# Kernel tuning notes

Hardware: AMD Instinct MI355X
Metric: run time of the kernel (lower is better)

The kernel has to match this reference:

```python
import jax, jax.numpy as jnp
import numpy as np

H = 8   # n_heads
C = 2   # top-k scale factor: topk = int(C * log(L))


def setup_inputs() -> dict:
    key = jax.random.key(0)
    k1, k2, k3 = jax.random.split(key, 3)
    B, L, D = 16, 512, 4096  # L == D // H required by the original broadcasting
    Q = jax.random.normal(k1, (B, L, D), dtype=jnp.float32)
    K = jax.random.normal(k2, (B, L, D), dtype=jnp.float32)
    V = jax.random.normal(k3, (B, L, D), dtype=jnp.float32)
    return {"Q": Q, "K": K, "V": V}


def _autocorrelation(Q, K, V):
    B, L, D = Q.shape
    d = D // H
    # [B,L,D] -> [B,H,L,d]
    q = Q.reshape(B, L, H, d).transpose(0, 2, 1, 3)
    k = K.reshape(B, L, H, d).transpose(0, 2, 1, 3)
    v = V.reshape(B, L, H, d).transpose(0, 2, 1, 3)
    # FFT-based autocorrelation along the time axis (per head, per channel)
    qf = jnp.fft.fft(q, axis=2)
    kf = jnp.fft.fft(k, axis=2)
    corr = jnp.fft.ifft(qf * jnp.conj(kf), axis=2).real  # [B,H,L,d]
    topk = int(C * np.log(L))  # static: 12 for L=512
    # top-k delays per (batch, head, channel): move L to last axis
    w, idx = jax.lax.top_k(corr.transpose(0, 1, 3, 2), topk)  # [B,H,d,topk]
    w = jax.nn.softmax(w, axis=-1)
    pos = jnp.arange(L)[:, None]  # [L,1]
    out = jnp.zeros_like(v)       # [B,H,L,d]
    # small fixed loop over topk ~ O(log L) delays: gather + scale + accumulate
    for i in range(topk):
        g = jnp.minimum(idx[:, :, None, :, i] + pos, L - 1)        # [B,H,L,d]
        out = out + w[:, :, None, :, i] * jnp.take_along_axis(v, g, axis=2)
    return out.transpose(0, 2, 1, 3).reshape(B, L, D)


def reference(Q, K, V):
    return _autocorrelation(Q, K, V)
```

## Files before the change

kernel.cpp:

```cpp
#include <hip/hip_runtime.h>
#include <stdint.h>

#define L_LEN 512
#define D_DIM 4096
#define H_NUM 8
#define B_NUM 16
#define TOPK  12

typedef float f32x4 __attribute__((ext_vector_type(4)));


#define QA(G) (qbase + (((((uint32_t)(G)) & 127u) + ((((uint32_t)(G)) & 127u) >> 3)) << 4))

#define MAC4x16(QA_, QB_, QC_, QD_, QE_, KK_) do {                            \
    acc0  = fmaf(QA_.x, KK_.x, acc0);  acc0  = fmaf(QA_.y, KK_.y, acc0);      \
    acc0  = fmaf(QA_.z, KK_.z, acc0);  acc0  = fmaf(QA_.w, KK_.w, acc0);      \
    acc1  = fmaf(QA_.y, KK_.x, acc1);  acc1  = fmaf(QA_.z, KK_.y, acc1);      \
    acc1  = fmaf(QA_.w, KK_.z, acc1);  acc1  = fmaf(QB_.x, KK_.w, acc1);      \
    acc2  = fmaf(QA_.z, KK_.x, acc2);  acc2  = fmaf(QA_.w, KK_.y, acc2);      \
    acc2  = fmaf(QB_.x, KK_.z, acc2);  acc2  = fmaf(QB_.y, KK_.w, acc2);      \
    acc3  = fmaf(QA_.w, KK_.x, acc3);  acc3  = fmaf(QB_.x, KK_.y, acc3);      \
    acc3  = fmaf(QB_.y, KK_.z, acc3);  acc3  = fmaf(QB_.z, KK_.w, acc3);      \
    acc4  = fmaf(QB_.x, KK_.x, acc4);  acc4  = fmaf(QB_.y, KK_.y, acc4);      \
    acc4  = fmaf(QB_.z, KK_.z, acc4);  acc4  = fmaf(QB_.w, KK_.w, acc4);      \
    acc5  = fmaf(QB_.y, KK_.x, acc5);  acc5  = fmaf(QB_.z, KK_.y, acc5);      \
    acc5  = fmaf(QB_.w, KK_.z, acc5);  acc5  = fmaf(QC_.x, KK_.w, acc5);      \
    acc6  = fmaf(QB_.z, KK_.x, acc6);  acc6  = fmaf(QB_.w, KK_.y, acc6);      \
    acc6  = fmaf(QC_.x, KK_.z, acc6);  acc6  = fmaf(QC_.y, KK_.w, acc6);      \
    acc7  = fmaf(QB_.w, KK_.x, acc7);  acc7  = fmaf(QC_.x, KK_.y, acc7);      \
    acc7  = fmaf(QC_.y, KK_.z, acc7);  acc7  = fmaf(QC_.z, KK_.w, acc7);      \
    acc8  = fmaf(QC_.x, KK_.x, acc8);  acc8  = fmaf(QC_.y, KK_.y, acc8);      \
    acc8  = fmaf(QC_.z, KK_.z, acc8);  acc8  = fmaf(QC_.w, KK_.w, acc8);      \
    acc9  = fmaf(QC_.y, KK_.x, acc9);  acc9  = fmaf(QC_.z, KK_.y, acc9);      \
    acc9  = fmaf(QC_.w, KK_.z, acc9);  acc9  = fmaf(QD_.x, KK_.w, acc9);      \
    acc10 = fmaf(QC_.z, KK_.x, acc10); acc10 = fmaf(QC_.w, KK_.y, acc10);     \
    acc10 = fmaf(QD_.x, KK_.z, acc10); acc10 = fmaf(QD_.y, KK_.w, acc10);     \
    acc11 = fmaf(QC_.w, KK_.x, acc11); acc11 = fmaf(QD_.x, KK_.y, acc11);     \
    acc11 = fmaf(QD_.y, KK_.z, acc11); acc11 = fmaf(QD_.z, KK_.w, acc11);     \
    acc12 = fmaf(QD_.x, KK_.x, acc12); acc12 = fmaf(QD_.y, KK_.y, acc12);     \
    acc12 = fmaf(QD_.z, KK_.z, acc12); acc12 = fmaf(QD_.w, KK_.w, acc12);     \
    acc13 = fmaf(QD_.y, KK_.x, acc13); acc13 = fmaf(QD_.z, KK_.y, acc13);     \
    acc13 = fmaf(QD_.w, KK_.z, acc13); acc13 = fmaf(QE_.x, KK_.w, acc13);     \
    acc14 = fmaf(QD_.z, KK_.x, acc14); acc14 = fmaf(QD_.w, KK_.y, acc14);     \
    acc14 = fmaf(QE_.x, KK_.z, acc14); acc14 = fmaf(QE_.y, KK_.w, acc14);     \
    acc15 = fmaf(QD_.w, KK_.x, acc15); acc15 = fmaf(QE_.x, KK_.y, acc15);     \
    acc15 = fmaf(QE_.y, KK_.z, acc15); acc15 = fmaf(QE_.z, KK_.w, acc15);     \
  } while (0)

#define ITERX(A0,A1,A2,A3, B0,B1,B2,B3, C0,C1,C2,C3) do {                    \
    const uint32_t a0_ = QA(gnext);                                          \
    const uint32_t a1_ = QA(gnext + 1);                                      \
    const uint32_t a2_ = QA(gnext + 2);                                      \
    const uint32_t a3_ = QA(gnext + 3);                                      \
    asm volatile(                                                            \
      "ds_read_b128 %0, %8\n\t"                                              \
      "ds_read_b128 %1, %9\n\t"                                              \
      "ds_read_b128 %2, %10\n\t"                                             \
      "ds_read_b128 %3, %11\n\t"                                             \
      "ds_read_b128 %4, %12\n\t"                                             \
      "ds_read_b128 %5, %12 offset:16\n\t"                                   \
      "ds_read_b128 %6, %12 offset:32\n\t"                                   \
      "ds_read_b128 %7, %12 offset:48\n\t"                                   \
      "s_waitcnt lgkmcnt(0)"                                                 \
      : "=&v"(C0), "=&v"(C1), "=&v"(C2), "=&v"(C3),                          \
        "=&v"(k0), "=&v"(k1), "=&v"(k2), "=&v"(k3)                           \
      : "v"(a0_), "v"(a1_), "v"(a2_), "v"(a3_), "v"(kptr)                    \
      : "memory");                                                           \
    MAC4x16(A0, A1, A2, A3, B0, k0);                                         \
    MAC4x16(A1, A2, A3, B0, B1, k1);                                         \
    MAC4x16(A2, A3, B0, B1, B2, k2);                                         \
    MAC4x16(A3, B0, B1, B2, B3, k3);                                         \
    gnext += 4; kptr += 64;                                                  \
  } while (0)

__global__ __launch_bounds__(256, 4) void corr_topk_kernel(
    const float* __restrict__ Q, const float* __restrict__ K,
    float* __restrict__ ws_w, int* __restrict__ ws_i)
{
  __shared__ __align__(16) float qs[8][576];
  __shared__ __align__(16) float ks[8][512];

  const int tid = threadIdx.x;
  const int bid = blockIdx.x;
  const int work = (bid & 7) * 1024 + (bid >> 3);
  const int bh   = work >> 6;
  const int c0   = (work & 63) * 8;

  const size_t base = (size_t)(bh >> 3) * (size_t)(L_LEN * D_DIM)
                    + (size_t)(bh & 7) * 512 + c0;

  #pragma unroll
  for (int rep = 0; rep < 4; ++rep) {
    const int idx  = rep * 256 + tid;
    const int t    = idx >> 1;
    const int half = idx & 1;
    const float4 qv = *(const float4*)(Q + base + (size_t)t * D_DIM + half * 4);
    const float4 kv = *(const float4*)(K + base + (size_t)t * D_DIM + half * 4);
    const int g  = t >> 2;
    const int pw = ((g + (g >> 3)) << 2) | (t & 3);
    const int cb = half * 4;
    const float qa[4] = {qv.x, qv.y, qv.z, qv.w};
    const float ka[4] = {kv.x, kv.y, kv.z, kv.w};
    #pragma unroll
    for (int j = 0; j < 4; ++j) {
      qs[cb + j][pw] = qa[j];
      ks[cb + j][t]  = ka[j];
    }
  }
  __syncthreads();

  const int wv   = tid >> 6;
  const int lane = tid & 63;
  const int m    = lane & 31;
  const int ch   = wv * 2 + (lane >> 5);
  const int tau0 = m * 16;
  const int gq   = m * 4;

  const uint32_t qbase = (uint32_t)(uintptr_t)(&qs[ch][0]);
  uint32_t       kptr  = (uint32_t)(uintptr_t)(&ks[ch][0]);

  float acc0  = 0.f, acc1  = 0.f, acc2  = 0.f, acc3  = 0.f;
  float acc4  = 0.f, acc5  = 0.f, acc6  = 0.f, acc7  = 0.f;
  float acc8  = 0.f, acc9  = 0.f, acc10 = 0.f, acc11 = 0.f;
  float acc12 = 0.f, acc13 = 0.f, acc14 = 0.f, acc15 = 0.f;
  f32x4 wA0, wA1, wA2, wA3, wB0, wB1, wB2, wB3, wC0, wC1, wC2, wC3;
  f32x4 k0, k1, k2, k3;

  {
    const uint32_t p0 = QA(gq),     p1 = QA(gq + 1);
    const uint32_t p2 = QA(gq + 2), p3 = QA(gq + 3);
    const uint32_t p4 = QA(gq + 4), p5 = QA(gq + 5);
    const uint32_t p6 = QA(gq + 6), p7 = QA(gq + 7);
    asm volatile(
      "ds_read_b128 %0, %8\n\t"
      "ds_read_b128 %1, %9\n\t"
      "ds_read_b128 %2, %10\n\t"
      "ds_read_b128 %3, %11\n\t"
      "ds_read_b128 %4, %12\n\t"
      "ds_read_b128 %5, %13\n\t"
      "ds_read_b128 %6, %14\n\t"
      "ds_read_b128 %7, %15\n\t"
      "s_waitcnt lgkmcnt(0)"
      : "=&v"(wA0), "=&v"(wA1), "=&v"(wA2), "=&v"(wA3),
        "=&v"(wB0), "=&v"(wB1), "=&v"(wB2), "=&v"(wB3)
      : "v"(p0), "v"(p1), "v"(p2), "v"(p3), "v"(p4), "v"(p5), "v"(p6), "v"(p7)
      : "memory");
  }

  uint32_t gnext = (uint32_t)(gq + 8);

  #pragma unroll 1
  for (int i = 0; i < 30; i += 3) {
    ITERX(wA0,wA1,wA2,wA3, wB0,wB1,wB2,wB3, wC0,wC1,wC2,wC3);
    ITERX(wB0,wB1,wB2,wB3, wC0,wC1,wC2,wC3, wA0,wA1,wA2,wA3);
    ITERX(wC0,wC1,wC2,wC3, wA0,wA1,wA2,wA3, wB0,wB1,wB2,wB3);
  }
  ITERX(wA0,wA1,wA2,wA3, wB0,wB1,wB2,wB3, wC0,wC1,wC2,wC3);
  ITERX(wB0,wB1,wB2,wB3, wC0,wC1,wC2,wC3, wA0,wA1,wA2,wA3);

  float acc[16] = {acc0, acc1, acc2,  acc3,  acc4,  acc5,  acc6,  acc7,
                   acc8, acc9, acc10, acc11, acc12, acc13, acc14, acc15};

  float bv[TOPK]; int bi[TOPK];
  #pragma unroll
  for (int s = 0; s < TOPK; ++s) {
    float lv = acc[0]; int li = 0;
    #pragma unroll
    for (int i = 1; i < 16; ++i) if (acc[i] > lv) { lv = acc[i]; li = i; }
    int gi = tau0 + li;
    #pragma unroll
    for (int off = 16; off >= 1; off >>= 1) {
      const float ov = __shfl_xor(lv, off, 32);
      const int   oi = __shfl_xor(gi, off, 32);
      if (ov > lv || (ov == lv && oi < gi)) { lv = ov; gi = oi; }
    }
    bv[s] = lv; bi[s] = gi;
    const int slot = gi - tau0;
    #pragma unroll
    for (int i = 0; i < 16; ++i) acc[i] = (slot == i) ? -3.4e38f : acc[i];
  }

  float e[TOPK]; float sum = 0.f;
  #pragma unroll
  for (int s = 0; s < TOPK; ++s) { e[s] = expf(bv[s] - bv[0]); sum += e[s]; }
  const float inv = 1.f / sum;

  if (m == 0) {
    const int g = (bh * 512 + c0 + ch) * TOPK;
    #pragma unroll
    for (int s = 0; s < TOPK; ++s) { ws_w[g + s] = e[s] * inv; ws_i[g + s] = bi[s]; }
  }
}

__global__ __launch_bounds__(512, 8) void gather_kernel(
    const float* __restrict__ V, const float* __restrict__ ws_w,
    const int* __restrict__ ws_i, float* __restrict__ out)
{
  __shared__ __align__(16) float vs[512][16];

  const int tid = threadIdx.x;
  const int bid = blockIdx.x;
  const int work = (bid & 7) * 512 + (bid >> 3);
  const int b  = work >> 8;
  const int dg = work & 255;
  const int d0 = dg * 16;
  const int h  = d0 >> 9;
  const int c0 = d0 & 511;

  const size_t vcol = (size_t)b * (size_t)(L_LEN * D_DIM) + d0;

  const int cl   = tid & 15;
  const int tsub = tid >> 4;

  const int ra = tid >> 2;
  const int qa = (tid & 3) * 4;

  float4 stga;
  stga = *(const float4*)(V + vcol + (size_t)(384 + ra) * D_DIM + qa);

  const int g = ((b * 8 + h) * 512 + c0 + cl) * TOPK;
  float w[TOPK]; int r0[TOPK];
  #pragma unroll
  for (int s = 0; s < TOPK; ++s) { w[s] = ws_w[g + s]; r0[s] = ws_i[g + s]; }

  const size_t ob = vcol + cl;

  #pragma unroll 1
  for (int ph = 3; ph >= 0; --ph) {
    *(float4*)(&vs[ph * 128 + ra][qa]) = stga;
    if (ph > 0) {
      stga = *(const float4*)(V + vcol + (size_t)((ph - 1) * 128 + ra) * D_DIM + qa);
    }
    asm volatile("s_waitcnt lgkmcnt(0)" ::: "memory");
    __builtin_amdgcn_s_barrier();
    asm volatile("" ::: "memory");

    #pragma unroll
    for (int j = 0; j < 4; ++j) {
      const int t = ph * 128 + j * 32 + tsub;
      float a = 0.f;
      #pragma unroll
      for (int s = 0; s < TOPK; ++s) {
        int r = r0[s] + t;
        r = r > (L_LEN - 1) ? (L_LEN - 1) : r;
        a = fmaf(w[s], vs[r][cl], a);
      }
      out[ob + (size_t)t * D_DIM] = a;
    }
  }
}

extern "C" void kernel_launch(void* const* d_in, const int* in_sizes, int n_in,
                              void* d_out, int out_size, void* d_ws, size_t ws_size,
                              hipStream_t stream)
{
  const float* Q = (const float*)d_in[0];
  const float* K = (const float*)d_in[1];
  const float* V = (const float*)d_in[2];
  float* out = (float*)d_out;

  float* ws_w = (float*)d_ws;
  int*   ws_i = (int*)((char*)d_ws + (size_t)B_NUM * H_NUM * 512 * TOPK * sizeof(float));

  corr_topk_kernel<<<dim3(B_NUM * H_NUM * 64), dim3(256), 0, stream>>>(Q, K, ws_w, ws_i);
  gather_kernel<<<dim3(B_NUM * 256), dim3(512), 0, stream>>>(V, ws_w, ws_i, out);
}
```

Before: 791.4 us.

## Double per-thread lag tile in correlation and emit two rows per gather thread

The correlation kernel now has each thread accumulate 32 lags instead of 16, using 16 lanes per channel and 128-thread blocks. The Q register window slides across four vector groups, and each loaded K vector feeds twice as many FMAs, cutting LDS traffic per FMA. The top-k shuffle reduction shrinks to 16 lanes. The gather kernel computes two consecutive output rows per thread and reuses the clamped index, with a padded extra LDS row holding a copy of row 511 so the clamp stays correct. The risk is higher register pressure and lower occupancy in the correlation kernel.

```diff
diff --git a/kernel.cpp b/kernel.cpp
--- a/kernel.cpp
+++ b/kernel.cpp
@@ -12,7 +12,7 @@
 
 #define QA(G) (qbase + (((((uint32_t)(G)) & 127u) + ((((uint32_t)(G)) & 127u) >> 3)) << 4))
 
-#define MAC4x16(QA_, QB_, QC_, QD_, QE_, KK_) do {                            \
+#define MACLO(QA_, QB_, QC_, QD_, QE_, KK_) do {                              \
     acc0  = fmaf(QA_.x, KK_.x, acc0);  acc0  = fmaf(QA_.y, KK_.y, acc0);      \
     acc0  = fmaf(QA_.z, KK_.z, acc0);  acc0  = fmaf(QA_.w, KK_.w, acc0);      \
     acc1  = fmaf(QA_.y, KK_.x, acc1);  acc1  = fmaf(QA_.z, KK_.y, acc1);      \
@@ -47,33 +47,68 @@
     acc15 = fmaf(QE_.y, KK_.z, acc15); acc15 = fmaf(QE_.z, KK_.w, acc15);     \
   } while (0)
 
-#define ITERX(A0,A1,A2,A3, B0,B1,B2,B3, C0,C1,C2,C3) do {                    \
-    const uint32_t a0_ = QA(gnext);                                          \
-    const uint32_t a1_ = QA(gnext + 1);                                      \
-    const uint32_t a2_ = QA(gnext + 2);                                      \
-    const uint32_t a3_ = QA(gnext + 3);                                      \
-    asm volatile(                                                            \
-      "ds_read_b128 %0, %8\n\t"                                              \
-      "ds_read_b128 %1, %9\n\t"                                              \
-      "ds_read_b128 %2, %10\n\t"                                             \
-      "ds_read_b128 %3, %11\n\t"                                             \
-      "ds_read_b128 %4, %12\n\t"                                             \
-      "ds_read_b128 %5, %12 offset:16\n\t"                                   \
-      "ds_read_b128 %6, %12 offset:32\n\t"                                   \
-      "ds_read_b128 %7, %12 offset:48\n\t"                                   \
-      "s_waitcnt lgkmcnt(0)"                                                 \
-      : "=&v"(C0), "=&v"(C1), "=&v"(C2), "=&v"(C3),                          \
-        "=&v"(k0), "=&v"(k1), "=&v"(k2), "=&v"(k3)                           \
-      : "v"(a0_), "v"(a1_), "v"(a2_), "v"(a3_), "v"(kptr)                    \
-      : "memory");                                                           \
-    MAC4x16(A0, A1, A2, A3, B0, k0);                                         \
-    MAC4x16(A1, A2, A3, B0, B1, k1);                                         \
-    MAC4x16(A2, A3, B0, B1, B2, k2);                                         \
-    MAC4x16(A3, B0, B1, B2, B3, k3);                                         \
-    gnext += 4; kptr += 64;                                                  \
+#define MACHI(QA_, QB_, QC_, QD_, QE_, KK_) do {                              \
+    acc16 = fmaf(QA_.x, KK_.x, acc16); acc16 = fmaf(QA_.y, KK_.y, acc16);     \
+    acc16 = fmaf(QA_.z, KK_.z, acc16); acc16 = fmaf(QA_.w, KK_.w, acc16);     \
+    acc17 = fmaf(QA_.y, KK_.x, acc17); acc17 = fmaf(QA_.z, KK_.y, acc17);     \
+    acc17 = fmaf(QA_.w, KK_.z, acc17); acc17 = fmaf(QB_.x, KK_.w, acc17);     \
+    acc18 = fmaf(QA_.z, KK_.x, acc18); acc18 = fmaf(QA_.w, KK_.y, acc18);     \
+    acc18 = fmaf(QB_.x, KK_.z, acc18); acc18 = fmaf(QB_.y, KK_.w, acc18);     \
+    acc19 = fmaf(QA_.w, KK_.x, acc19); acc19 = fmaf(QB_.x, KK_.y, acc19);     \
+    acc19 = fmaf(QB_.y, KK_.z, acc19); acc19 = fmaf(QB_.z, KK_.w, acc19);     \
+    acc20 = fmaf(QB_.x, KK_.x, acc20); acc20 = fmaf(QB_.y, KK_.y, acc20);     \
+    acc20 = fmaf(QB_.z, KK_.z, acc20); acc20 = fmaf(QB_.w, KK_.w, acc20);     \
+    acc21 = fmaf(QB_.y, KK_.x, acc21); acc21 = fmaf(QB_.z, KK_.y, acc21);     \
+    acc21 = fmaf(QB_.w, KK_.z, acc21); acc21 = fmaf(QC_.x, KK_.w, acc21);     \
+    acc22 = fmaf(QB_.z, KK_.x, acc22); acc22 = fmaf(QB_.w, KK_.y, acc22);     \
+    acc22 = fmaf(QC_.x, KK_.z, acc22); acc22 = fmaf(QC_.y, KK_.w, acc22);     \
+    acc23 = fmaf(QB_.w, KK_.x, acc23); acc23 = fmaf(QC_.x, KK_.y, acc23);     \
+    acc23 = fmaf(QC_.y, KK_.z, acc23); acc23 = fmaf(QC_.z, KK_.w, acc23);     \
+    acc24 = fmaf(QC_.x, KK_.x, acc24); acc24 = fmaf(QC_.y, KK_.y, acc24);     \
+    acc24 = fmaf(QC_.z, KK_.z, acc24); acc24 = fmaf(QC_.w, KK_.w, acc24);     \
+    acc25 = fmaf(QC_.y, KK_.x, acc25); acc25 = fmaf(QC_.z, KK_.y, acc25);     \
+    acc25 = fmaf(QC_.w, KK_.z, acc25); acc25 = fmaf(QD_.x, KK_.w, acc25);     \
+    acc26 = fmaf(QC_.z, KK_.x, acc26); acc26 = fmaf(QC_.w, KK_.y, acc26);     \
+    acc26 = fmaf(QD_.x, KK_.z, acc26); acc26 = fmaf(QD_.y, KK_.w, acc26);     \
+    acc27 = fmaf(QC_.w, KK_.x, acc27); acc27 = fmaf(QD_.x, KK_.y, acc27);     \
+    acc27 = fmaf(QD_.y, KK_.z, acc27); acc27 = fmaf(QD_.z, KK_.w, acc27);     \
+    acc28 = fmaf(QD_.x, KK_.x, acc28); acc28 = fmaf(QD_.y, KK_.y, acc28);     \
+    acc28 = fmaf(QD_.z, KK_.z, acc28); acc28 = fmaf(QD_.w, KK_.w, acc28);     \
+    acc29 = fmaf(QD_.y, KK_.x, acc29); acc29 = fmaf(QD_.z, KK_.y, acc29);     \
+    acc29 = fmaf(QD_.w, KK_.z, acc29); acc29 = fmaf(QE_.x, KK_.w, acc29);     \
+    acc30 = fmaf(QD_.z, KK_.x, acc30); acc30 = fmaf(QD_.w, KK_.y, acc30);     \
+    acc30 = fmaf(QE_.x, KK_.z, acc30); acc30 = fmaf(QE_.y, KK_.w, acc30);     \
+    acc31 = fmaf(QD_.w, KK_.x, acc31); acc31 = fmaf(QE_.x, KK_.y, acc31);     \
+    acc31 = fmaf(QE_.y, KK_.z, acc31); acc31 = fmaf(QE_.z, KK_.w, acc31);     \
   } while (0)
 
-__global__ __launch_bounds__(256, 4) void corr_topk_kernel(
+#define ITER32(L0,L1,L2,L3,L4,L5,L6,L7,L8,L9,L10,L11, X0,X1,X2,X3) do {       \
+    const uint32_t a0_ = QA(gnext);                                           \
+    const uint32_t a1_ = QA(gnext + 1);                                       \
+    const uint32_t a2_ = QA(gnext + 2);                                       \
+    const uint32_t a3_ = QA(gnext + 3);                                       \
+    asm volatile(                                                             \
+      "ds_read_b128 %0, %8\n\t"                                               \
+      "ds_read_b128 %1, %9\n\t"                                               \
+      "ds_read_b128 %2, %10\n\t"                                              \
+      "ds_read_b128 %3, %11\n\t"                                              \
+      "ds_read_b128 %4, %12\n\t"                                              \
+      "ds_read_b128 %5, %12 offset:16\n\t"                                    \
+      "ds_read_b128 %6, %12 offset:32\n\t"                                    \
+      "ds_read_b128 %7, %12 offset:48\n\t"                                    \
+      "s_waitcnt lgkmcnt(0)"                                                  \
+      : "=&v"(X0), "=&v"(X1), "=&v"(X2), "=&v"(X3),                           \
+        "=&v"(k0), "=&v"(k1), "=&v"(k2), "=&v"(k3)                            \
+      : "v"(a0_), "v"(a1_), "v"(a2_), "v"(a3_), "v"(kptr)                     \
+      : "memory");                                                            \
+    MACLO(L0, L1, L2, L3, L4, k0);  MACHI(L4, L5, L6, L7, L8, k0);            \
+    MACLO(L1, L2, L3, L4, L5, k1);  MACHI(L5, L6, L7, L8, L9, k1);            \
+    MACLO(L2, L3, L4, L5, L6, k2);  MACHI(L6, L7, L8, L9, L10, k2);           \
+    MACLO(L3, L4, L5, L6, L7, k3);  MACHI(L7, L8, L9, L10, L11, k3);          \
+    gnext += 4; kptr += 64;                                                   \
+  } while (0)
+
+__global__ __launch_bounds__(128, 4) void corr_topk_kernel(
     const float* __restrict__ Q, const float* __restrict__ K,
     float* __restrict__ ws_w, int* __restrict__ ws_i)
 {
@@ -90,8 +125,8 @@
                     + (size_t)(bh & 7) * 512 + c0;
 
   #pragma unroll
-  for (int rep = 0; rep < 4; ++rep) {
-    const int idx  = rep * 256 + tid;
+  for (int rep = 0; rep < 8; ++rep) {
+    const int idx  = rep * 128 + tid;
     const int t    = idx >> 1;
     const int half = idx & 1;
     const float4 qv = *(const float4*)(Q + base + (size_t)t * D_DIM + half * 4);
@@ -111,10 +146,10 @@
 
   const int wv   = tid >> 6;
   const int lane = tid & 63;
-  const int m    = lane & 31;
-  const int ch   = wv * 2 + (lane >> 5);
-  const int tau0 = m * 16;
-  const int gq   = m * 4;
+  const int m    = lane & 15;
+  const int ch   = wv * 4 + (lane >> 4);
+  const int tau0 = m * 32;
+  const uint32_t gq = (uint32_t)(m * 8);
 
   const uint32_t qbase = (uint32_t)(uintptr_t)(&qs[ch][0]);
   uint32_t       kptr  = (uint32_t)(uintptr_t)(&ks[ch][0]);
@@ -123,61 +158,82 @@
   float acc4  = 0.f, acc5  = 0.f, acc6  = 0.f, acc7  = 0.f;
   float acc8  = 0.f, acc9  = 0.f, acc10 = 0.f, acc11 = 0.f;
   float acc12 = 0.f, acc13 = 0.f, acc14 = 0.f, acc15 = 0.f;
-  f32x4 wA0, wA1, wA2, wA3, wB0, wB1, wB2, wB3, wC0, wC1, wC2, wC3;
+  float acc16 = 0.f, acc17 = 0.f, acc18 = 0.f, acc19 = 0.f;
+  float acc20 = 0.f, acc21 = 0.f, acc22 = 0.f, acc23 = 0.f;
+  float acc24 = 0.f, acc25 = 0.f, acc26 = 0.f, acc27 = 0.f;
+  float acc28 = 0.f, acc29 = 0.f, acc30 = 0.f, acc31 = 0.f;
+  f32x4 A0, A1, A2, A3, B0, B1, B2, B3, C0, C1, C2, C3, D0, D1, D2, D3;
   f32x4 k0, k1, k2, k3;
 
   {
-    const uint32_t p0 = QA(gq),     p1 = QA(gq + 1);
-    const uint32_t p2 = QA(gq + 2), p3 = QA(gq + 3);
-    const uint32_t p4 = QA(gq + 4), p5 = QA(gq + 5);
-    const uint32_t p6 = QA(gq + 6), p7 = QA(gq + 7);
+    const uint32_t p0 = QA(gq),      p1 = QA(gq + 1);
+    const uint32_t p2 = QA(gq + 2),  p3 = QA(gq + 3);
+    const uint32_t p4 = QA(gq + 4),  p5 = QA(gq + 5);
+    const uint32_t p6 = QA(gq + 6),  p7 = QA(gq + 7);
+    const uint32_t p8 = QA(gq + 8),  p9 = QA(gq + 9);
+    const uint32_t pa = QA(gq + 10), pb = QA(gq + 11);
     asm volatile(
-      "ds_read_b128 %0, %8\n\t"
-      "ds_read_b128 %1, %9\n\t"
-      "ds_read_b128 %2, %10\n\t"
-      "ds_read_b128 %3, %11\n\t"
-      "ds_read_b128 %4, %12\n\t"
-      "ds_read_b128 %5, %13\n\t"
-      "ds_read_b128 %6, %14\n\t"
-      "ds_read_b128 %7, %15\n\t"
+      "ds_read_b128 %0, %12\n\t"
+      "ds_read_b128 %1, %13\n\t"
+      "ds_read_b128 %2, %14\n\t"
+      "ds_read_b128 %3, %15\n\t"
+      "ds_read_b128 %4, %16\n\t"
+      "ds_read_b128 %5, %17\n\t"
+      "ds_read_b128 %6, %18\n\t"
+      "ds_read_b128 %7, %19\n\t"
+      "ds_read_b128 %8, %20\n\t"
+      "ds_read_b128 %9, %21\n\t"
+      "ds_read_b128 %10, %22\n\t"
+      "ds_read_b128 %11, %23"
+      : "=&v"(A0), "=&v"(A1), "=&v"(A2), "=&v"(A3),
+        "=&v"(B0), "=&v"(B1), "=&v"(B2), "=&v"(B3),
+        "=&v"(C0), "=&v"(C1), "=&v"(C2), "=&v"(C3)
+      : "v"(p0), "v"(p1), "v"(p2), "v"(p3), "v"(p4), "v"(p5),
+        "v"(p6), "v"(p7), "v"(p8), "v"(p9), "v"(pa), "v"(pb)
+      : "memory");
+    asm volatile(
+      "ds_read_b128 %0, %4\n\t"
+      "ds_read_b128 %1, %4 offset:16\n\t"
+      "ds_read_b128 %2, %4 offset:32\n\t"
+      "ds_read_b128 %3, %4 offset:48\n\t"
       "s_waitcnt lgkmcnt(0)"
-      : "=&v"(wA0), "=&v"(wA1), "=&v"(wA2), "=&v"(wA3),
-        "=&v"(wB0), "=&v"(wB1), "=&v"(wB2), "=&v"(wB3)
-      : "v"(p0), "v"(p1), "v"(p2), "v"(p3), "v"(p4), "v"(p5), "v"(p6), "v"(p7)
+      : "=&v"(k0), "=&v"(k1), "=&v"(k2), "=&v"(k3)
+      : "v"(kptr)
       : "memory");
   }
 
-  uint32_t gnext = (uint32_t)(gq + 8);
+  uint32_t gnext = gq + 12;
 
   #pragma unroll 1
-  for (int i = 0; i < 30; i += 3) {
-    ITERX(wA0,wA1,wA2,wA3, wB0,wB1,wB2,wB3, wC0,wC1,wC2,wC3);
-    ITERX(wB0,wB1,wB2,wB3, wC0,wC1,wC2,wC3, wA0,wA1,wA2,wA3);
-    ITERX(wC0,wC1,wC2,wC3, wA0,wA1,wA2,wA3, wB0,wB1,wB2,wB3);
-  }
-  ITERX(wA0,wA1,wA2,wA3, wB0,wB1,wB2,wB3, wC0,wC1,wC2,wC3);
-  ITERX(wB0,wB1,wB2,wB3, wC0,wC1,wC2,wC3, wA0,wA1,wA2,wA3);
-
-  float acc[16] = {acc0, acc1, acc2,  acc3,  acc4,  acc5,  acc6,  acc7,
-                   acc8, acc9, acc10, acc11, acc12, acc13, acc14, acc15};
+  for (int it = 0; it < 8; ++it) {
+    ITER32(A0,A1,A2,A3, B0,B1,B2,B3, C0,C1,C2,C3, D0,D1,D2,D3);
+    ITER32(B0,B1,B2,B3, C0,C1,C2,C3, D0,D1,D2,D3, A0,A1,A2,A3);
+    ITER32(C0,C1,C2,C3, D0,D1,D2,D3, A0,A1,A2,A3, B0,B1,B2,B3);
+    ITER32(D0,D1,D2,D3, A0,A1,A2,A3, B0,B1,B2,B3, C0,C1,C2,C3);
+  }
+
+  float acc[32] = {acc0,  acc1,  acc2,  acc3,  acc4,  acc5,  acc6,  acc7,
+                   acc8,  acc9,  acc10, acc11, acc12, acc13, acc14, acc15,
+                   acc16, acc17, acc18, acc19, acc20, acc21, acc22, acc23,
+                   acc24, acc25, acc26, acc27, acc28, acc29, acc30, acc31};
 
   float bv[TOPK]; int bi[TOPK];
   #pragma unroll
   for (int s = 0; s < TOPK; ++s) {
     float lv = acc[0]; int li = 0;
     #pragma unroll
-    for (int i = 1; i < 16; ++i) if (acc[i] > lv) { lv = acc[i]; li = i; }
+    for (int i = 1; i < 32; ++i) if (acc[i] > lv) { lv = acc[i]; li = i; }
     int gi = tau0 + li;
     #pragma unroll
-    for (int off = 16; off >= 1; off >>= 1) {
-      const float ov = __shfl_xor(lv, off, 32);
-      const int   oi = __shfl_xor(gi, off, 32);
+    for (int off = 8; off >= 1; off >>= 1) {
+      const float ov = __shfl_xor(lv, off, 16);
+      const int   oi = __shfl_xor(gi, off, 16);
       if (ov > lv || (ov == lv && oi < gi)) { lv = ov; gi = oi; }
     }
     bv[s] = lv; bi[s] = gi;
     const int slot = gi - tau0;
     #pragma unroll
-    for (int i = 0; i < 16; ++i) acc[i] = (slot == i) ? -3.4e38f : acc[i];
+    for (int i = 0; i < 32; ++i) acc[i] = (slot == i) ? -3.4e38f : acc[i];
   }
 
   float e[TOPK]; float sum = 0.f;
@@ -196,7 +252,7 @@
     const float* __restrict__ V, const float* __restrict__ ws_w,
     const int* __restrict__ ws_i, float* __restrict__ out)
 {
-  __shared__ __align__(16) float vs[512][16];
+  __shared__ __align__(16) float vs[513][16];
 
   const int tid = threadIdx.x;
   const int bid = blockIdx.x;
@@ -209,8 +265,8 @@
 
   const size_t vcol = (size_t)b * (size_t)(L_LEN * D_DIM) + d0;
 
-  const int cl   = tid & 15;
-  const int tsub = tid >> 4;
+  const int cl = tid & 15;
+  const int tp = tid >> 4;
 
   const int ra = tid >> 2;
   const int qa = (tid & 3) * 4;
@@ -228,6 +284,8 @@
   #pragma unroll 1
   for (int ph = 3; ph >= 0; --ph) {
     *(float4*)(&vs[ph * 128 + ra][qa]) = stga;
+    if (ph == 3 && ra == 127)
+      *(float4*)(&vs[512][qa]) = stga;
     if (ph > 0) {
       stga = *(const float4*)(V + vcol + (size_t)((ph - 1) * 128 + ra) * D_DIM + qa);
     }
@@ -236,16 +294,20 @@
     asm volatile("" ::: "memory");
 
     #pragma unroll
-    for (int j = 0; j < 4; ++j) {
-      const int t = ph * 128 + j * 32 + tsub;
-      float a = 0.f;
+    for (int j = 0; j < 2; ++j) {
+      const int tb = ph * 128 + j * 64 + tp * 2;
+      float a0 = 0.f, a1 = 0.f;
       #pragma unroll
       for (int s = 0; s < TOPK; ++s) {
-        int r = r0[s] + t;
+        int r = r0[s] + tb;
         r = r > (L_LEN - 1) ? (L_LEN - 1) : r;
-        a = fmaf(w[s], vs[r][cl], a);
+        const float v0 = vs[r][cl];
+        const float v1 = vs[r + 1][cl];
+        a0 = fmaf(w[s], v0, a0);
+        a1 = fmaf(w[s], v1, a1);
       }
-      out[ob + (size_t)t * D_DIM] = a;
+      out[ob + (size_t)tb * D_DIM]       = a0;
+      out[ob + (size_t)(tb + 1) * D_DIM] = a1;
     }
   }
 }
@@ -262,6 +324,6 @@
   float* ws_w = (float*)d_ws;
   int*   ws_i = (int*)((char*)d_ws + (size_t)B_NUM * H_NUM * 512 * TOPK * sizeof(float));
 
-  corr_topk_kernel<<<dim3(B_NUM * H_NUM * 64), dim3(256), 0, stream>>>(Q, K, ws_w, ws_i);
+  corr_topk_kernel<<<dim3(B_NUM * H_NUM * 64), dim3(128), 0, stream>>>(Q, K, ws_w, ws_i);
   gather_kernel<<<dim3(B_NUM * 256), dim3(512), 0, stream>>>(V, ws_w, ws_i, out);
 }
```

Measured after the change: 736.8 us. 1.07x faster.
